# Kernel tuning notes

Measured on AMD Instinct MI355X. Metric: run time of the kernel, lower is better.

Reference implementation:

```python
import jax, jax.numpy as jnp
import numpy as np


def setup_inputs() -> dict:
    key = jax.random.key(0)
    k1, k2, k3, k4 = jax.random.split(key, 4)
    B, E, R, D = 1024, 8192, 16, 128
    head = jax.random.randint(k1, (B,), 0, E)
    tail = jax.random.randint(k2, (B,), 0, E)
    entity_embeddings = jax.random.normal(k3, (E, D), dtype=jnp.float32)
    rule_embeddings = jax.random.normal(k4, (R, D), dtype=jnp.float32)
    return {
        "head": head,
        "tail": tail,
        "query_relation": 3,
        "depth": 1,
        "entity_embeddings": entity_embeddings,
        "rule_embeddings": rule_embeddings,
    }


def reference(head, tail, query_relation, depth, entity_embeddings, rule_embeddings):
    # NeuralTheoremProver.prove at depth == 1 (deepest runnable config):
    #   score[b] = sum_r mean_z  s1[r,b,z] * s2[b,z]
    #   s1[r,b,z] = -|| e[head_b] + rule_r - e[z] ||_2       (base_case of prove #1)
    #   s2[b,z]   = -|| e[z] + rule_q - e[tail_b] ||_2       (base_case of prove #2)
    # Squared L2 is expanded via dot products so we never materialize [R,B,E,D].
    E_tab = entity_embeddings                      # [E, D]
    h = E_tab[head]                                # [B, D]
    t = E_tab[tail]                                # [B, D]
    hh = jnp.sum(h * h, axis=-1)                   # [B]
    tt = jnp.sum(t * t, axis=-1)                   # [B]
    zz = jnp.sum(E_tab * E_tab, axis=-1)           # [E]
    rr = jnp.sum(rule_embeddings * rule_embeddings, axis=-1)  # [R]

    hr = h @ rule_embeddings.T                     # [B, R]
    hz = h @ E_tab.T                               # [B, E]
    rz = rule_embeddings @ E_tab.T                 # [R, E]

    # ||h + r - z||^2 = hh + rr + zz + 2 h.r - 2 h.z - 2 r.z   -> [R, B, E]
    sq1 = (hh[None, :, None] + rr[:, None, None] + zz[None, None, :]
           + 2.0 * hr.T[:, :, None] - 2.0 * hz[None, :, :] - 2.0 * rz[:, None, :])
    S1 = -jnp.sum(jnp.sqrt(jnp.maximum(sq1, 0.0)), axis=0)     # [B, E] = sum_r s1

    q = rule_embeddings[query_relation]            # [D]
    qq = jnp.sum(q * q)
    zq = E_tab @ q                                 # [E]
    zt = t @ E_tab.T                               # [B, E]
    qt = t @ q                                     # [B]
    # ||z + q - t||^2 = zz + qq + tt + 2 z.q - 2 z.t - 2 q.t   -> [B, E]
    sq2 = zz[None, :] + qq + tt[:, None] + 2.0 * zq[None, :] - 2.0 * zt - 2.0 * qt[:, None]
    s2 = -jnp.sqrt(jnp.maximum(sq2, 0.0))          # [B, E]

    return jnp.mean(S1 * s2, axis=1)               # [B]
```

## Files before the change

### kernel.cpp

```cpp
#include <hip/hip_runtime.h>


typedef __attribute__((ext_vector_type(8))) short short8;
typedef __attribute__((ext_vector_type(4))) float f32x4;

__device__ inline unsigned short f2bf(float f) {
  unsigned int u = __float_as_uint(f);
  u += 0x7fffu + ((u >> 16) & 1u);
  return (unsigned short)(u >> 16);
}

__device__ inline float wred64(float v) {
#pragma unroll
  for (int o = 32; o > 0; o >>= 1) v += __shfl_xor(v, o, 64);
  return v;
}

__global__ void ntp_zero(float* out, int n) {
  int i = blockIdx.x * blockDim.x + threadIdx.x;
  if (i < n) out[i] = 0.f;
}

__global__ __launch_bounds__(64) void ntp_pre_entity(
    const float* __restrict__ Etab, const float* __restrict__ rules,
    const int* __restrict__ qrelp, unsigned short* __restrict__ Ebf,
    float* __restrict__ Gz, float* __restrict__ G2) {
  const int z = blockIdx.x, tid = threadIdx.x;
  const float* e = Etab + (size_t)z * 128;
  float e0 = e[tid], e1 = e[tid + 64];
  Ebf[(size_t)z * 128 + tid]      = f2bf(e0);
  Ebf[(size_t)z * 128 + tid + 64] = f2bf(e1);
  float zz = wred64(e0 * e0 + e1 * e1);
  const int qrel = qrelp[0];
  const float* q = rules + (size_t)qrel * 128;
  float q0 = q[tid], q1 = q[tid + 64];
  float qq = wred64(q0 * q0 + q1 * q1);
  float zq = wred64(e0 * q0 + e1 * q1);
  if (tid == 0) G2[z] = zz + 2.f * zq + qq;
  for (int r = 0; r < 16; ++r) {
    const float* rp = rules + (size_t)r * 128;
    float r0 = rp[tid], r1 = rp[tid + 64];
    float rz = wred64(e0 * r0 + e1 * r1);
    if (tid == 0) Gz[(size_t)z * 16 + r] = zz - 2.f * rz;
  }
}

__global__ __launch_bounds__(64) void ntp_pre_b(
    const float* __restrict__ Etab, const float* __restrict__ rules,
    const int* __restrict__ head, const int* __restrict__ tail,
    const int* __restrict__ qrelp, unsigned short* __restrict__ Hbf,
    unsigned short* __restrict__ Tbf, float* __restrict__ C1,
    float* __restrict__ C2) {
  const int b = blockIdx.x, tid = threadIdx.x;
  const int hi = head[b], ti = tail[b];
  const float* h = Etab + (size_t)hi * 128;
  const float* t = Etab + (size_t)ti * 128;
  float h0 = h[tid], h1 = h[tid + 64];
  float t0 = t[tid], t1 = t[tid + 64];
  Hbf[(size_t)b * 128 + tid]      = f2bf(h0);
  Hbf[(size_t)b * 128 + tid + 64] = f2bf(h1);
  Tbf[(size_t)b * 128 + tid]      = f2bf(t0);
  Tbf[(size_t)b * 128 + tid + 64] = f2bf(t1);
  float hh = wred64(h0 * h0 + h1 * h1);
  float tt = wred64(t0 * t0 + t1 * t1);
  const int qrel = qrelp[0];
  const float* q = rules + (size_t)qrel * 128;
  float q0 = q[tid], q1 = q[tid + 64];
  float qt = wred64(t0 * q0 + t1 * q1);
  if (tid == 0) C2[b] = tt - 2.f * qt;
  for (int r = 0; r < 16; ++r) {
    const float* rp = rules + (size_t)r * 128;
    float r0 = rp[tid], r1 = rp[tid + 64];
    float rr = wred64(r0 * r0 + r1 * r1);
    float hr = wred64(h0 * r0 + h1 * r1);
    if (tid == 0) C1[(size_t)b * 16 + r] = hh + rr + 2.f * hr;
  }
}

__global__ __launch_bounds__(256, 4) void ntp_main(
    const unsigned short* __restrict__ Ebf, const unsigned short* __restrict__ Hbf,
    const unsigned short* __restrict__ Tbf, const float* __restrict__ Gz,
    const float* __restrict__ G2, const float* __restrict__ C1,
    const float* __restrict__ C2, float* __restrict__ out, int Ecount) {
  __shared__ __align__(16) unsigned short sEz[32][136];
  __shared__ __align__(16) float sGz[32][36];
  __shared__ __align__(16) float sG2[32];
  __shared__ __align__(16) float sC1[32][16];
  __shared__ __align__(16) float sC2[32];

  const int tid   = threadIdx.x;
  const int lane  = tid & 63, wave = tid >> 6;
  const int bhalf = wave >> 1, zhalf = wave & 1;
  const int quad  = lane >> 4, lm = lane & 15;
  const int b_base = blockIdx.x * 32;
  const int z_base = blockIdx.y * 256;

  if (tid < 128) {
    *reinterpret_cast<f32x4*>(&sC1[tid >> 2][(tid & 3) * 4]) =
        *reinterpret_cast<const f32x4*>(&C1[(size_t)(b_base + (tid >> 2)) * 16 + (tid & 3) * 4]);
  }
  if (tid < 32) sC2[tid] = C2[b_base + tid];

  short8 hfrag[4], tfrag[4];
  {
    const size_t brow = (size_t)(b_base + bhalf * 16 + lm) * 128 + quad * 8;
    const unsigned short* hp = Hbf + brow;
    const unsigned short* tp = Tbf + brow;
#pragma unroll
    for (int k4 = 0; k4 < 4; ++k4) {
      hfrag[k4] = *reinterpret_cast<const short8*>(hp + k4 * 32);
      tfrag[k4] = *reinterpret_cast<const short8*>(tp + k4 * 32);
    }
  }

  const int z_loc = zhalf * 16 + lm;
  const float scale = 1.0f / (float)Ecount;
  f32x4 acc_out = {0.f, 0.f, 0.f, 0.f};

  for (int c = 0; c < 8; ++c) {
    const int z0 = z_base + c * 32;
    __syncthreads();
    {
      int u = tid;
#pragma unroll
      for (int rep = 0; rep < 2; ++rep, u += 256) {
        int row = u >> 4, col = u & 15;
        *reinterpret_cast<short8*>(&sEz[row][col * 8]) =
            *reinterpret_cast<const short8*>(Ebf + (size_t)(z0 + row) * 128 + col * 8);
      }
    }
    if (tid < 128) {
      int row = tid >> 2, col = tid & 3;
      *reinterpret_cast<f32x4*>(&sGz[row][col * 4]) =
          *reinterpret_cast<const f32x4*>(&Gz[(size_t)(z0 + row) * 16 + col * 4]);
    }
    if (tid < 32) sG2[tid] = G2[z0 + tid];
    __syncthreads();

    f32x4 acc_hz = {0.f, 0.f, 0.f, 0.f};
    f32x4 acc_zt = {0.f, 0.f, 0.f, 0.f};
#pragma unroll
    for (int k4 = 0; k4 < 4; ++k4) {
      short8 ef = *reinterpret_cast<const short8*>(&sEz[z_loc][k4 * 32 + quad * 8]);
      acc_hz = __builtin_amdgcn_mfma_f32_16x16x32_bf16(hfrag[k4], ef, acc_hz, 0, 0, 0);
      acc_zt = __builtin_amdgcn_mfma_f32_16x16x32_bf16(tfrag[k4], ef, acc_zt, 0, 0, 0);
    }

    f32x4 gr[4];
#pragma unroll
    for (int i = 0; i < 4; ++i)
      gr[i] = *reinterpret_cast<const f32x4*>(&sGz[z_loc][i * 4]);
    const float g2v = sG2[z_loc];
#pragma unroll
    for (int reg = 0; reg < 4; ++reg) {
      const int b_loc = bhalf * 16 + quad * 4 + reg;
      const float hz = acc_hz[reg], zt = acc_zt[reg];
      const float sq2 = g2v + sC2[b_loc] - 2.f * zt;
      const float s2 = __builtin_amdgcn_sqrtf(fmaxf(sq2, 0.f));
      f32x4 c1q[4];
#pragma unroll
      for (int i = 0; i < 4; ++i)
        c1q[i] = *reinterpret_cast<const f32x4*>(&sC1[b_loc][i * 4]);
      const float m2hz = -2.f * hz;
      float S1 = 0.f;
#pragma unroll
      for (int r = 0; r < 16; ++r) {
        const float sq1 = (c1q[r >> 2][r & 3] + gr[r >> 2][r & 3]) + m2hz;
        S1 += __builtin_amdgcn_sqrtf(fmaxf(sq1, 0.f));
      }
      acc_out[reg] += S1 * s2;
    }
  }

#pragma unroll
  for (int reg = 0; reg < 4; ++reg) {
    float v = acc_out[reg];
    v += __shfl_xor(v, 1, 16);
    v += __shfl_xor(v, 2, 16);
    v += __shfl_xor(v, 4, 16);
    v += __shfl_xor(v, 8, 16);
    if (lm == 0)
      atomicAdd(&out[b_base + bhalf * 16 + quad * 4 + reg], v * scale);
  }
}

extern "C" void kernel_launch(void* const* d_in, const int* in_sizes, int n_in,
                              void* d_out, int out_size, void* d_ws, size_t ws_size,
                              hipStream_t stream) {
  const int* head  = (const int*)d_in[0];
  const int* tail  = (const int*)d_in[1];
  const int* qrel  = (const int*)d_in[2];
  const float* Etab  = (const float*)d_in[4];
  const float* rules = (const float*)d_in[5];
  const int B = in_sizes[0];
  const int E = in_sizes[4] / 128;
  float* out = (float*)d_out;

  char* ws = (char*)d_ws;
  unsigned short* Ebf = (unsigned short*)ws;
  unsigned short* Hbf = (unsigned short*)(ws + (size_t)E * 256);
  unsigned short* Tbf = Hbf + (size_t)B * 128;
  float* Gz = (float*)(ws + (size_t)E * 256 + (size_t)B * 512);
  float* G2 = Gz + (size_t)E * 16;
  float* C1 = G2 + E;
  float* C2 = C1 + (size_t)B * 16;

  ntp_zero<<<(B + 255) / 256, 256, 0, stream>>>(out, B);
  ntp_pre_entity<<<E, 64, 0, stream>>>(Etab, rules, qrel, Ebf, Gz, G2);
  ntp_pre_b<<<B, 64, 0, stream>>>(Etab, rules, head, tail, qrel, Hbf, Tbf, C1, C2);
  ntp_main<<<dim3(B / 32, E / 256), 256, 0, stream>>>(Ebf, Hbf, Tbf, Gz, G2, C1,
                                                      C2, out, E);
}
```

Before: 123.7 us.

## Fuse preprocessing kernels into one and hoist per-row constants into registers

Merges the zeroing, entity precompute and batch precompute kernels into one launch. Each thread now computes one (row, rule) dot product serially with vector loads, replacing the 64-lane shuffle reductions repeated for every rule. In the main kernel, the per-batch-row C1/C2 constants are loaded from shared memory once into registers instead of every chunk iteration, and the occupancy hint drops from 4 to 2 blocks per unit to make room for the extra registers. This saves launch overhead and shared-memory traffic at the cost of register pressure and possibly lower occupancy.

```diff
diff --git a/kernel.cpp b/kernel.cpp
--- a/kernel.cpp
+++ b/kernel.cpp
@@ -10,74 +10,78 @@
   return (unsigned short)(u >> 16);
 }
 
-__device__ inline float wred64(float v) {
-#pragma unroll
-  for (int o = 32; o > 0; o >>= 1) v += __shfl_xor(v, o, 64);
-  return v;
-}
-
-__global__ void ntp_zero(float* out, int n) {
-  int i = blockIdx.x * blockDim.x + threadIdx.x;
-  if (i < n) out[i] = 0.f;
-}
-
-__global__ __launch_bounds__(64) void ntp_pre_entity(
-    const float* __restrict__ Etab, const float* __restrict__ rules,
-    const int* __restrict__ qrelp, unsigned short* __restrict__ Ebf,
-    float* __restrict__ Gz, float* __restrict__ G2) {
-  const int z = blockIdx.x, tid = threadIdx.x;
-  const float* e = Etab + (size_t)z * 128;
-  float e0 = e[tid], e1 = e[tid + 64];
-  Ebf[(size_t)z * 128 + tid]      = f2bf(e0);
-  Ebf[(size_t)z * 128 + tid + 64] = f2bf(e1);
-  float zz = wred64(e0 * e0 + e1 * e1);
-  const int qrel = qrelp[0];
-  const float* q = rules + (size_t)qrel * 128;
-  float q0 = q[tid], q1 = q[tid + 64];
-  float qq = wred64(q0 * q0 + q1 * q1);
-  float zq = wred64(e0 * q0 + e1 * q1);
-  if (tid == 0) G2[z] = zz + 2.f * zq + qq;
-  for (int r = 0; r < 16; ++r) {
-    const float* rp = rules + (size_t)r * 128;
-    float r0 = rp[tid], r1 = rp[tid + 64];
-    float rz = wred64(e0 * r0 + e1 * r1);
-    if (tid == 0) Gz[(size_t)z * 16 + r] = zz - 2.f * rz;
-  }
-}
-
-__global__ __launch_bounds__(64) void ntp_pre_b(
+__global__ __launch_bounds__(256) void ntp_pre(
     const float* __restrict__ Etab, const float* __restrict__ rules,
     const int* __restrict__ head, const int* __restrict__ tail,
-    const int* __restrict__ qrelp, unsigned short* __restrict__ Hbf,
-    unsigned short* __restrict__ Tbf, float* __restrict__ C1,
-    float* __restrict__ C2) {
-  const int b = blockIdx.x, tid = threadIdx.x;
-  const int hi = head[b], ti = tail[b];
-  const float* h = Etab + (size_t)hi * 128;
-  const float* t = Etab + (size_t)ti * 128;
-  float h0 = h[tid], h1 = h[tid + 64];
-  float t0 = t[tid], t1 = t[tid + 64];
-  Hbf[(size_t)b * 128 + tid]      = f2bf(h0);
-  Hbf[(size_t)b * 128 + tid + 64] = f2bf(h1);
-  Tbf[(size_t)b * 128 + tid]      = f2bf(t0);
-  Tbf[(size_t)b * 128 + tid + 64] = f2bf(t1);
-  float hh = wred64(h0 * h0 + h1 * h1);
-  float tt = wred64(t0 * t0 + t1 * t1);
+    const int* __restrict__ qrelp, unsigned short* __restrict__ Ebf,
+    unsigned short* __restrict__ Hbf, unsigned short* __restrict__ Tbf,
+    float* __restrict__ Gz, float* __restrict__ G2, float* __restrict__ C1,
+    float* __restrict__ C2, float* __restrict__ out, int nEB) {
+  const int tid = threadIdx.x;
+  const int gl = tid >> 4;
+  const int r  = tid & 15;
   const int qrel = qrelp[0];
-  const float* q = rules + (size_t)qrel * 128;
-  float q0 = q[tid], q1 = q[tid + 64];
-  float qt = wred64(t0 * q0 + t1 * q1);
-  if (tid == 0) C2[b] = tt - 2.f * qt;
-  for (int r = 0; r < 16; ++r) {
-    const float* rp = rules + (size_t)r * 128;
-    float r0 = rp[tid], r1 = rp[tid + 64];
-    float rr = wred64(r0 * r0 + r1 * r1);
-    float hr = wred64(h0 * r0 + h1 * r1);
-    if (tid == 0) C1[(size_t)b * 16 + r] = hh + rr + 2.f * hr;
-  }
-}
-
-__global__ __launch_bounds__(256, 4) void ntp_main(
+  const float* rp = rules + (size_t)r * 128;
+
+  if ((int)blockIdx.x < nEB) {
+    const int z = blockIdx.x * 16 + gl;
+    const float* ez = Etab + (size_t)z * 128;
+    float rz = 0.f, zz = 0.f, rr = 0.f;
+#pragma unroll
+    for (int k = 0; k < 128; k += 4) {
+      f32x4 ev = *reinterpret_cast<const f32x4*>(ez + k);
+      f32x4 rv = *reinterpret_cast<const f32x4*>(rp + k);
+#pragma unroll
+      for (int j = 0; j < 4; ++j) {
+        rz += ev[j] * rv[j];
+        zz += ev[j] * ev[j];
+        rr += rv[j] * rv[j];
+      }
+    }
+    Gz[(size_t)z * 16 + r] = zz - 2.f * rz;
+    if (r == qrel) G2[z] = zz + 2.f * rz + rr;
+    const float* src = ez + r * 8;
+    short8 o;
+#pragma unroll
+    for (int j = 0; j < 8; ++j) o[j] = (short)f2bf(src[j]);
+    *reinterpret_cast<short8*>(Ebf + (size_t)z * 128 + r * 8) = o;
+  } else {
+    const int b = (blockIdx.x - nEB) * 16 + gl;
+    const int hi = head[b], ti = tail[b];
+    const float* hp = Etab + (size_t)hi * 128;
+    const float* tp = Etab + (size_t)ti * 128;
+    float hr = 0.f, tq = 0.f, hh = 0.f, tt = 0.f, rr = 0.f;
+#pragma unroll
+    for (int k = 0; k < 128; k += 4) {
+      f32x4 hv = *reinterpret_cast<const f32x4*>(hp + k);
+      f32x4 tv = *reinterpret_cast<const f32x4*>(tp + k);
+      f32x4 rv = *reinterpret_cast<const f32x4*>(rp + k);
+#pragma unroll
+      for (int j = 0; j < 4; ++j) {
+        hr += hv[j] * rv[j];
+        tq += tv[j] * rv[j];
+        hh += hv[j] * hv[j];
+        tt += tv[j] * tv[j];
+        rr += rv[j] * rv[j];
+      }
+    }
+    C1[(size_t)b * 16 + r] = hh + rr + 2.f * hr;
+    if (r == qrel) C2[b] = tt - 2.f * tq;
+    if (r == 0) out[b] = 0.f;
+    short8 oh, ot;
+    const float* hsrc = hp + r * 8;
+    const float* tsrc = tp + r * 8;
+#pragma unroll
+    for (int j = 0; j < 8; ++j) {
+      oh[j] = (short)f2bf(hsrc[j]);
+      ot[j] = (short)f2bf(tsrc[j]);
+    }
+    *reinterpret_cast<short8*>(Hbf + (size_t)b * 128 + r * 8) = oh;
+    *reinterpret_cast<short8*>(Tbf + (size_t)b * 128 + r * 8) = ot;
+  }
+}
+
+__global__ __launch_bounds__(256, 2) void ntp_main(
     const unsigned short* __restrict__ Ebf, const unsigned short* __restrict__ Hbf,
     const unsigned short* __restrict__ Tbf, const float* __restrict__ Gz,
     const float* __restrict__ G2, const float* __restrict__ C1,
@@ -113,6 +117,18 @@
     }
   }
 
+  __syncthreads();
+  f32x4 c1q[4][4];
+  float c2v[4];
+#pragma unroll
+  for (int reg = 0; reg < 4; ++reg) {
+    const int b_loc = bhalf * 16 + quad * 4 + reg;
+#pragma unroll
+    for (int i = 0; i < 4; ++i)
+      c1q[reg][i] = *reinterpret_cast<const f32x4*>(&sC1[b_loc][i * 4]);
+    c2v[reg] = sC2[b_loc];
+  }
+
   const int z_loc = zhalf * 16 + lm;
   const float scale = 1.0f / (float)Ecount;
   f32x4 acc_out = {0.f, 0.f, 0.f, 0.f};
@@ -153,21 +169,18 @@
     const float g2v = sG2[z_loc];
 #pragma unroll
     for (int reg = 0; reg < 4; ++reg) {
-      const int b_loc = bhalf * 16 + quad * 4 + reg;
       const float hz = acc_hz[reg], zt = acc_zt[reg];
-      const float sq2 = g2v + sC2[b_loc] - 2.f * zt;
+      const float sq2 = g2v + c2v[reg] - 2.f * zt;
       const float s2 = __builtin_amdgcn_sqrtf(fmaxf(sq2, 0.f));
-      f32x4 c1q[4];
-#pragma unroll
-      for (int i = 0; i < 4; ++i)
-        c1q[i] = *reinterpret_cast<const f32x4*>(&sC1[b_loc][i * 4]);
       const float m2hz = -2.f * hz;
       float S1 = 0.f;
 #pragma unroll
-      for (int r = 0; r < 16; ++r) {
-        const float sq1 = (c1q[r >> 2][r & 3] + gr[r >> 2][r & 3]) + m2hz;
-        S1 += __builtin_amdgcn_sqrtf(fmaxf(sq1, 0.f));
-      }
+      for (int i = 0; i < 4; ++i)
+#pragma unroll
+        for (int j = 0; j < 4; ++j) {
+          const float sq1 = (c1q[reg][i][j] + gr[i][j]) + m2hz;
+          S1 += __builtin_amdgcn_sqrtf(fmaxf(sq1, 0.f));
+        }
       acc_out[reg] += S1 * s2;
     }
   }
@@ -205,9 +218,10 @@
   float* C1 = G2 + E;
   float* C2 = C1 + (size_t)B * 16;
 
-  ntp_zero<<<(B + 255) / 256, 256, 0, stream>>>(out, B);
-  ntp_pre_entity<<<E, 64, 0, stream>>>(Etab, rules, qrel, Ebf, Gz, G2);
-  ntp_pre_b<<<B, 64, 0, stream>>>(Etab, rules, head, tail, qrel, Hbf, Tbf, C1, C2);
+  const int nEB = E / 16;
+  const int nBB = B / 16;
+  ntp_pre<<<nEB + nBB, 256, 0, stream>>>(Etab, rules, head, tail, qrel, Ebf,
+                                         Hbf, Tbf, Gz, G2, C1, C2, out, nEB);
   ntp_main<<<dim3(B / 32, E / 256), 256, 0, stream>>>(Ebf, Hbf, Tbf, Gz, G2, C1,
                                                       C2, out, E);
 }
```

After: 120.4 us. -2.6%, faster.
